# Optimization experiments

Hardware: AMD Instinct MI355X
Metric: run time of the kernel (lower is better)

The kernel has to match this reference:

```python
import jax, jax.numpy as jnp
import numpy as np

N = 100000
E = 1600000
IN_DIM, HID_DIM, OUT_DIM = 128, 64, 128


def glorot(key, shape):
    lim = float(np.sqrt(6.0 / (shape[0] + shape[1])))
    return jax.random.uniform(key, shape, jnp.float32, -lim, lim)


def setup_inputs() -> dict:
    key = jax.random.key(0)
    k1, k2, k3, k4, k5 = jax.random.split(key, 5)
    x = jax.random.normal(k1, (N, IN_DIM), jnp.float32)
    edge_index = jax.random.randint(k2, (2, E), 0, N, jnp.int64)
    edge_weight = jax.random.uniform(k3, (E,), jnp.float32)
    W1 = glorot(k4, (IN_DIM, HID_DIM))
    b1 = jnp.zeros((HID_DIM,), jnp.float32)
    W2 = glorot(k5, (HID_DIM, OUT_DIM))
    b2 = jnp.zeros((OUT_DIM,), jnp.float32)
    return {"x": x, "edge_index": edge_index, "edge_weight": edge_weight,
            "W1": W1, "b1": b1, "W2": W2, "b2": b2}


def gcn_norm(edge_index, edge_weight, num_nodes):
    # add self-loops with weight 1 (PyG GCNConv default)
    loops = jnp.arange(num_nodes, dtype=edge_index.dtype)
    row = jnp.concatenate([edge_index[0], loops])
    col = jnp.concatenate([edge_index[1], loops])
    w = jnp.concatenate([edge_weight, jnp.ones((num_nodes,), edge_weight.dtype)])
    deg = jax.ops.segment_sum(w, col, num_segments=num_nodes)  # in-degree of targets
    dinv = jnp.where(deg > 0, jax.lax.rsqrt(deg), 0.0)
    norm = dinv[row] * w * dinv[col]  # [E+N]
    return row, col, norm


def gcn_conv(x, row, col, norm, W, b, num_nodes):
    h = x @ W                                   # [N, D_out]
    msg = h[row] * norm[:, None]                # [E+N, D_out] gather + scale
    out = jax.ops.segment_sum(msg, col, num_segments=num_nodes)  # scatter-add
    return out + b


def reference(x, edge_index, edge_weight, W1, b1, W2, b2):
    row, col, norm = gcn_norm(edge_index, edge_weight, N)
    h = jax.nn.relu(gcn_conv(x, row, col, norm, W1, b1, N))
    out = gcn_conv(h, row, col, norm, W2, b2, N)
    return out
```

## Files before the change

kernel.cpp:

```cpp
#include <hip/hip_runtime.h>
#include <hip/hip_bf16.h>

typedef __hip_bfloat16 bf16;
typedef __attribute__((ext_vector_type(8))) short short8;
typedef __attribute__((ext_vector_type(4))) float f32x4;
typedef __attribute__((ext_vector_type(2))) unsigned uv2;
typedef __attribute__((ext_vector_type(4))) unsigned uv4;
union V8 { uint4 u; short8 v; };

__device__ __forceinline__ float bf2f(bf16 v) { return __bfloat162float(v); }
__device__ __forceinline__ float lo16(unsigned u) { return __uint_as_float((u & 0xffffu) << 16); }
__device__ __forceinline__ float hi16(unsigned u) { return __uint_as_float(u & 0xffff0000u); }
__device__ __forceinline__ unsigned short f2bfbits(float f) {
    return (unsigned short)(__hip_bfloat16_raw(__float2bfloat16(f)).x);
}
__device__ __forceinline__ unsigned pack2(float a, float b) {
    return (unsigned)f2bfbits(a) | ((unsigned)f2bfbits(b) << 16);
}

__device__ __forceinline__ float ldf(const void* p, size_t i, bool isbf) {
    return isbf ? bf2f(((const bf16*)p)[i]) : ((const float*)p)[i];
}
__device__ __forceinline__ int ldi(const void* p, size_t i, bool is64) {
    return is64 ? (int)((const long long*)p)[i] : ((const int*)p)[i];
}
__device__ __forceinline__ float sane(float v) {
    return (v == v && fabsf(v) < 1e30f) ? v : 0.f;
}

__device__ __forceinline__ uint2 nt_ld2(const uint2* p) {
    uv2 v = __builtin_nontemporal_load((const uv2*)p);
    return make_uint2(v.x, v.y);
}
__device__ __forceinline__ void nt_st4(uint4* p, uint4 v) {
    uv4 t; t.x = v.x; t.y = v.y; t.z = v.z; t.w = v.w;
    __builtin_nontemporal_store(t, (uv4*)p);
}

#define DC_CNT_SHIFT 44
#define DC_FIX_MASK  0xFFFFFFFFFFFULL
#define DC_FIX_SCALE 4194304.0f

__global__ void initk(unsigned long long* __restrict__ dc, int* __restrict__ hist,
                      int* __restrict__ bcnt, int n, int initdc,
                      const unsigned* __restrict__ w1w, const unsigned* __restrict__ eiw,
                      int* __restrict__ flags) {
    int i = blockIdx.x * blockDim.x + threadIdx.x;
    if (initdc && i < n) dc[i] = (unsigned long long)(1u << 22);
    if (i < 256) { hist[i] = 0; bcnt[i] = 0; }
    if (blockIdx.x == 0) {
        __shared__ int cnt[2];
        if (threadIdx.x < 2) cnt[threadIdx.x] = 0;
        __syncthreads();
        int c0 = 0;
        for (int j = threadIdx.x; j < 4096; j += 256) {
            unsigned u = w1w[j];
            unsigned e0 = (u >> 7) & 0xFFu, e1 = (u >> 23) & 0xFFu;
            if (e0 <= 125u && e1 <= 125u) c0++;
        }
        int c1 = 0;
        for (int j = threadIdx.x; j < 2048; j += 256)
            if (eiw[2 * j + 1] == 0u) c1++;
        atomicAdd(&cnt[0], c0);
        atomicAdd(&cnt[1], c1);
        __syncthreads();
        if (threadIdx.x == 0) {
            flags[0] = (cnt[0] >= 3072) ? 1 : 0;
            flags[1] = (cnt[1] >= 1024) ? 1 : 0;
        }
    }
}

__global__ void degcnt(const void* __restrict__ ei, const void* __restrict__ w,
                       unsigned long long* __restrict__ dc,
                       const int* __restrict__ flags, int e, int n) {
    const bool isbf = flags[0] != 0;
    const bool is64 = flags[1] != 0;
    int i = blockIdx.x * blockDim.x + threadIdx.x;
    if (i < e) {
        int c = ldi(ei, (size_t)e + i, is64);
        if ((unsigned)c < (unsigned)n) {
            float wv = sane(ldf(w, i, isbf));
            wv = fminf(fmaxf(wv, 0.f), 1024.f);
            unsigned long long pk = (1ULL << DC_CNT_SHIFT)
                                  + (unsigned long long)llrintf(wv * DC_FIX_SCALE);
            atomicAdd(&dc[c], pk);
        }
    }
}

__global__ __launch_bounds__(1024) void binA(const void* __restrict__ ei,
                                             const void* __restrict__ w,
                                             int* __restrict__ bcnt,
                                             uint2* __restrict__ stage,
                                             const int* __restrict__ flags,
                                             int e, int n, int k, int cap) {
    __shared__ uint2 recs[4096];
    __shared__ unsigned tgt[4096];
    __shared__ int lh[256], loff[256], lbase[256];
    const bool isbf = flags[0] != 0;
    const bool is64 = flags[1] != 0;
    const int t = threadIdx.x;
    if (t < 256) lh[t] = 0;
    __syncthreads();

    int b_[4], lr_[4], valid_[4];
    uint2 rec_[4];
    const int base = blockIdx.x * 4096;
#pragma unroll
    for (int u = 0; u < 4; ++u) {
        int i = base + u * 1024 + t;
        valid_[u] = 0;
        if (i < e) {
            int r = ldi(ei, (size_t)i, is64);
            int c = ldi(ei, (size_t)e + i, is64);
            if ((unsigned)c < (unsigned)n) {
                bool rv = (unsigned)r < (unsigned)n;
                float wv = rv ? sane(ldf(w, i, isbf)) : 0.f;
                int b = c >> k;
                unsigned cloc = (unsigned)(c - (b << k));
                rec_[u] = make_uint2((cloc << 20) | (rv ? (unsigned)r : 0u),
                                     __float_as_uint(wv));
                b_[u] = b;
                lr_[u] = atomicAdd(&lh[b], 1);
                valid_[u] = 1;
            }
        }
    }
    __syncthreads();

    if (t < 256) loff[t] = lh[t];
    __syncthreads();
    for (int off = 1; off < 256; off <<= 1) {
        int v = 0;
        if (t < 256 && t >= off) v = loff[t - off];
        __syncthreads();
        if (t < 256 && t >= off) loff[t] += v;
        __syncthreads();
    }
    if (t < 256) {
        int c = lh[t];
        loff[t] -= c;
        lbase[t] = (c > 0) ? atomicAdd(&bcnt[t], c) : 0;
    }
    __syncthreads();

#pragma unroll
    for (int u = 0; u < 4; ++u)
        if (valid_[u]) {
            int slot = loff[b_[u]] + lr_[u];
            recs[slot] = rec_[u];
            unsigned gi = (unsigned)(lbase[b_[u]] + lr_[u]);
            tgt[slot] = (gi < (unsigned)cap)
                          ? (unsigned)b_[u] * (unsigned)cap + gi
                          : 0xFFFFFFFFu;
        }
    __syncthreads();

    const int total = loff[255] + lh[255];
    for (int s = t; s < total; s += 1024) {
        unsigned g = tgt[s];
        if (g != 0xFFFFFFFFu) stage[g] = recs[s];
    }
}

__global__ __launch_bounds__(1024) void degcntB(const uint2* __restrict__ stage,
                                                const int* __restrict__ bcnt,
                                                unsigned long long* __restrict__ dc,
                                                int n, int k, int cap) {
    __shared__ unsigned long long dcl[4096];
    const int b  = blockIdx.x;
    const int lo = b << k;
    const int hi = min(n, lo + (1 << k));
    const int bs = hi - lo;
    const int t  = threadIdx.x;
    for (int j = t; j < bs; j += 1024)
        dcl[j] = (unsigned long long)(1u << 22);
    __syncthreads();
    const uint2* sb = stage + (size_t)b * cap;
    const int cnt_b = min(bcnt[b], cap);
    for (int s = t; s < cnt_b; s += 1024) {
        uint2 rec = sb[s];
        int cloc  = (int)(rec.x >> 20);
        float wv  = __uint_as_float(rec.y);
        wv = fminf(fmaxf(wv, 0.f), 1024.f);
        unsigned long long pk = (1ULL << DC_CNT_SHIFT)
                              + (unsigned long long)llrintf(wv * DC_FIX_SCALE);
        atomicAdd(&dcl[cloc], pk);
    }
    __syncthreads();
    for (int j = t; j < bs; j += 1024) dc[lo + j] = dcl[j];
}

__global__ __launch_bounds__(1024) void scan1(const unsigned long long* __restrict__ dc,
                                              int* __restrict__ rp,
                                              int* __restrict__ bsum, int n) {
    __shared__ int s[1024];
    int gid = blockIdx.x * 1024 + threadIdx.x;
    int v = (gid < n) ? (int)(((const unsigned*)dc)[2 * (size_t)gid + 1] >> (DC_CNT_SHIFT - 32)) : 0;
    s[threadIdx.x] = v;
    __syncthreads();
    for (int off = 1; off < 1024; off <<= 1) {
        int t = 0;
        if (threadIdx.x >= off) t = s[threadIdx.x - off];
        __syncthreads();
        if (threadIdx.x >= off) s[threadIdx.x] += t;
        __syncthreads();
    }
    if (gid < n) rp[gid] = s[threadIdx.x] - v;
    if (threadIdx.x == 1023) bsum[blockIdx.x] = s[1023];
}

__global__ __launch_bounds__(1024) void scan2(const int* __restrict__ bsum,
                                              int* __restrict__ bsx, int nb) {
    __shared__ int s[1024];
    int v = (threadIdx.x < nb) ? bsum[threadIdx.x] : 0;
    s[threadIdx.x] = v;
    __syncthreads();
    for (int off = 1; off < 1024; off <<= 1) {
        int t = 0;
        if (threadIdx.x >= off) t = s[threadIdx.x - off];
        __syncthreads();
        if (threadIdx.x >= off) s[threadIdx.x] += t;
        __syncthreads();
    }
    if (threadIdx.x < nb) bsx[threadIdx.x] = s[threadIdx.x] - v;
}

__global__ __launch_bounds__(1024) void scan3(int* __restrict__ rp, int* __restrict__ cursor,
                                              const int* __restrict__ bsx,
                                              unsigned long long* __restrict__ dc,
                                              int* __restrict__ hist,
                                              int n, int e) {
    __shared__ int lh[256];
    const int t = threadIdx.x;
    if (t < 256) lh[t] = 0;
    __syncthreads();
    int i = blockIdx.x * 1024 + t;
    if (i < n) {
        int v = rp[i] + bsx[i >> 10];
        rp[i] = v;
        cursor[i] = v;
        unsigned long long dv = dc[i];
        int c = (int)(dv >> DC_CNT_SHIFT);
        float d = (float)(dv & DC_FIX_MASK) * (1.0f / DC_FIX_SCALE);
        float di = d > 0.f ? rsqrtf(d) : 0.f;
        dc[i] = (dv & ~DC_FIX_MASK) | (unsigned long long)__float_as_uint(di);
        atomicAdd(&lh[min(c, 255)], 1);
    }
    __syncthreads();
    if (t < 256) {
        int c = lh[t];
        if (c > 0) atomicAdd(&hist[t], c);
    }
    if (i == 0) rp[n] = e;
}

__global__ void fill(const void* __restrict__ ei, const void* __restrict__ w,
                     int* __restrict__ cursor, uint2* __restrict__ epack,
                     const int* __restrict__ flags, int e, int n) {
    const bool isbf = flags[0] != 0;
    const bool is64 = flags[1] != 0;
    int i = blockIdx.x * blockDim.x + threadIdx.x;
    if (i < e) {
        int r = ldi(ei, (size_t)i, is64);
        int c = ldi(ei, (size_t)e + i, is64);
        if ((unsigned)c < (unsigned)n) {
            bool rv = (unsigned)r < (unsigned)n;
            float wv = rv ? sane(ldf(w, i, isbf)) : 0.f;
            int pos = atomicAdd(&cursor[c], 1);
            epack[pos] = make_uint2(rv ? (unsigned)r : 0u, __float_as_uint(wv));
        }
    }
}

__global__ __launch_bounds__(1024) void fillB(const int* __restrict__ rp,
                                              const uint2* __restrict__ stage,
                                              const int* __restrict__ bcnt,
                                              uint2* __restrict__ epack,
                                              int n, int k, int cap) {
    __shared__ int ncur[4096];
    const int b  = blockIdx.x;
    const int lo = b << k;
    const int hi = min(n, lo + (1 << k));
    const int t  = threadIdx.x;
    for (int j = t; j < hi - lo; j += 1024) ncur[j] = rp[lo + j];
    __syncthreads();
    const uint2* sb = stage + (size_t)b * cap;
    const int cnt_b = min(bcnt[b], cap);
    for (int s = t; s < cnt_b; s += 1024) {
        uint2 rec = sb[s];
        int cloc  = (int)(rec.x >> 20);
        unsigned r = rec.x & 0xFFFFFu;
        int pos = atomicAdd(&ncur[cloc], 1);
        epack[pos] = make_uint2(r, rec.y);
    }
}

__global__ void hscan(const int* __restrict__ hist, int* __restrict__ hcur) {
    __shared__ int s[256];
    int v = hist[threadIdx.x];
    s[threadIdx.x] = v;
    __syncthreads();
    for (int off = 1; off < 256; off <<= 1) {
        int t = 0;
        if (threadIdx.x >= off) t = s[threadIdx.x - off];
        __syncthreads();
        if (threadIdx.x >= off) s[threadIdx.x] += t;
        __syncthreads();
    }
    hcur[threadIdx.x] = s[threadIdx.x] - v;
}

__global__ __launch_bounds__(1024) void sortk(const unsigned long long* __restrict__ dc,
                                              int* __restrict__ hcur,
                                              int* __restrict__ order, int n) {
    __shared__ int lh[256];
    __shared__ int lbase[256];
    const int t = threadIdx.x;
    for (int b = t; b < 256; b += 1024) lh[b] = 0;
    __syncthreads();
    const int i = blockIdx.x * 1024 + t;
    int b = 0, lrank = 0;
    if (i < n) {
        b = min((int)(dc[i] >> DC_CNT_SHIFT), 255);
        lrank = atomicAdd(&lh[b], 1);
    }
    __syncthreads();
    for (int bb = t; bb < 256; bb += 1024) {
        int c = lh[bb];
        lbase[bb] = (c > 0) ? atomicAdd(&hcur[bb], c) : 0;
    }
    __syncthreads();
    if (i < n) order[lbase[b] + lrank] = i;
}

__global__ __launch_bounds__(256) void gemm1_mfma(const void* __restrict__ x,
                                                  const void* __restrict__ W1,
                                                  const float* __restrict__ dinvp,
                                                  const int* __restrict__ flags,
                                                  unsigned short* __restrict__ G1,
                                                  int n) {
    const bool isbf = flags[0] != 0;
    __shared__ uint4 bfr[16 * 64];
    for (int idx = threadIdx.x; idx < 16 * 64; idx += 256) {
        int lane = idx & 63, fr = idx >> 6;
        int ct = fr >> 2, ks = fr & 3;
        int k0 = ks * 32 + (lane >> 4) * 8;
        int col = ct * 16 + (lane & 15);
        unsigned short h[8];
#pragma unroll
        for (int j = 0; j < 8; ++j)
            h[j] = f2bfbits(ldf(W1, (size_t)(k0 + j) * 64 + col, isbf));
        bfr[idx] = make_uint4((unsigned)h[0] | ((unsigned)h[1] << 16),
                              (unsigned)h[2] | ((unsigned)h[3] << 16),
                              (unsigned)h[4] | ((unsigned)h[5] << 16),
                              (unsigned)h[6] | ((unsigned)h[7] << 16));
    }
    __syncthreads();

    const int lane = threadIdx.x & 63;
    const int m = lane & 15, q = lane >> 4;
    const int wid = (blockIdx.x * 256 + threadIdx.x) >> 6;
    const int nw  = (gridDim.x * 256) >> 6;
    const int nchunk = (n + 15) >> 4;

    for (int ch = wid; ch < nchunk; ch += nw) {
        const int row0 = ch * 16;
        const int rA = min(row0 + m, n - 1);
        V8 a[4];
        if (isbf) {
            const uint4* xr = (const uint4*)((const bf16*)x + (size_t)rA * 128);
#pragma unroll
            for (int ks = 0; ks < 4; ++ks) a[ks].u = xr[ks * 4 + q];
        } else {
            const float4* xr4 = (const float4*)((const float*)x + (size_t)rA * 128);
#pragma unroll
            for (int ks = 0; ks < 4; ++ks) {
                float4 v0 = xr4[ks * 8 + q * 2];
                float4 v1 = xr4[ks * 8 + q * 2 + 1];
                a[ks].u = make_uint4(pack2(v0.x, v0.y), pack2(v0.z, v0.w),
                                     pack2(v1.x, v1.y), pack2(v1.z, v1.w));
            }
        }
#pragma unroll
        for (int ct = 0; ct < 4; ++ct) {
            f32x4 acc = {0.f, 0.f, 0.f, 0.f};
#pragma unroll
            for (int ks = 0; ks < 4; ++ks) {
                V8 b; b.u = bfr[(ct * 4 + ks) * 64 + lane];
                acc = __builtin_amdgcn_mfma_f32_16x16x32_bf16(a[ks].v, b.v, acc, 0, 0, 0);
            }
#pragma unroll
            for (int r = 0; r < 4; ++r) {
                int row = row0 + q * 4 + r;
                if (row < n)
                    G1[(size_t)row * 64 + ct * 16 + m] = f2bfbits(dinvp[2 * (size_t)row] * acc[r]);
            }
        }
    }
}

__device__ __forceinline__ void gacc8(const int* __restrict__ rp,
                                      const uint2* __restrict__ epack,
                                      const uint4* __restrict__ Gv,
                                      int node, int sub, float acc[8]) {
    uint4 self = Gv[(size_t)node * 8 + sub];
    acc[0] = lo16(self.x); acc[1] = hi16(self.x);
    acc[2] = lo16(self.y); acc[3] = hi16(self.y);
    acc[4] = lo16(self.z); acc[5] = hi16(self.z);
    acc[6] = lo16(self.w); acc[7] = hi16(self.w);

    const int s0 = rp[node], s1 = rp[node + 1];
    const uint2 fb = make_uint2((unsigned)node, 0u);
    int idx = s0 + sub;
    uint2 ld = (idx < s1) ? nt_ld2(&epack[idx]) : fb;
    for (int base = s0; base < s1; base += 8) {
        int nidx = base + 8 + sub;
        uint2 nld = (nidx < s1) ? nt_ld2(&epack[nidx]) : fb;
        int rr[8]; float wv[8];
#pragma unroll
        for (int u = 0; u < 8; ++u) {
            rr[u] = __shfl((int)ld.x, u, 8);
            wv[u] = __uint_as_float((unsigned)__shfl((int)ld.y, u, 8));
        }
        uint4 gp[8];
#pragma unroll
        for (int u = 0; u < 8; ++u) gp[u] = Gv[(size_t)rr[u] * 8 + sub];
#pragma unroll
        for (int u = 0; u < 8; ++u) {
            acc[0] = fmaf(wv[u], lo16(gp[u].x), acc[0]);
            acc[1] = fmaf(wv[u], hi16(gp[u].x), acc[1]);
            acc[2] = fmaf(wv[u], lo16(gp[u].y), acc[2]);
            acc[3] = fmaf(wv[u], hi16(gp[u].y), acc[3]);
            acc[4] = fmaf(wv[u], lo16(gp[u].z), acc[4]);
            acc[5] = fmaf(wv[u], hi16(gp[u].z), acc[5]);
            acc[6] = fmaf(wv[u], lo16(gp[u].w), acc[6]);
            acc[7] = fmaf(wv[u], hi16(gp[u].w), acc[7]);
        }
        ld = nld;
    }
}

__global__ __launch_bounds__(256, 4) void agg1(const int* __restrict__ rp,
                                               const uint2* __restrict__ epack,
                                               const int* __restrict__ order,
                                               const uint4* __restrict__ G1v,
                                               const float* __restrict__ dinvp,
                                               const void* __restrict__ b1,
                                               const int* __restrict__ flags,
                                               uint4* __restrict__ G2v, int n) {
    const bool isbf = flags[0] != 0;
    const int sub = threadIdx.x & 7;
    const int g   = (blockIdx.x * 256 + threadIdx.x) >> 3;
    if (g >= n) return;
    const int node = order[g];

    float acc[8];
    gacc8(rp, epack, G1v, node, sub, acc);

    const float dv = dinvp[2 * (size_t)node];
    unsigned o[4];
#pragma unroll
    for (int t = 0; t < 4; ++t) {
        float h0 = dv * acc[2 * t]     + ldf(b1, 8 * sub + 2 * t, isbf);
        float h1 = dv * acc[2 * t + 1] + ldf(b1, 8 * sub + 2 * t + 1, isbf);
        h0 = h0 > 0.f ? h0 : 0.f;
        h1 = h1 > 0.f ? h1 : 0.f;
        o[t] = pack2(dv * h0, dv * h1);
    }
    nt_st4(&G2v[(size_t)node * 8 + sub], make_uint4(o[0], o[1], o[2], o[3]));
}

__global__ __launch_bounds__(256, 4) void agg2out(const int* __restrict__ rp,
                                                  const uint2* __restrict__ epack,
                                                  const int* __restrict__ order,
                                                  const uint4* __restrict__ G2v,
                                                  const float* __restrict__ dinvp,
                                                  const void* __restrict__ W2,
                                                  const void* __restrict__ b2,
                                                  const int* __restrict__ flags,
                                                  void* __restrict__ outp, int n) {
    const bool isbf = flags[0] != 0;
    __shared__ uint4 bfr[16 * 64];
    __shared__ float b2s[128];
    __shared__ uint4 tls[32 * 8];
    __shared__ int   nds[32];
    for (int idx = threadIdx.x; idx < 16 * 64; idx += 256) {
        int lane = idx & 63, fr = idx >> 6;
        int ct = fr >> 1, ks = fr & 1;
        int k0 = ks * 32 + (lane >> 4) * 8;
        int col = ct * 16 + (lane & 15);
        unsigned short h[8];
#pragma unroll
        for (int j = 0; j < 8; ++j)
            h[j] = f2bfbits(ldf(W2, (size_t)(k0 + j) * 128 + col, isbf));
        bfr[idx] = make_uint4((unsigned)h[0] | ((unsigned)h[1] << 16),
                              (unsigned)h[2] | ((unsigned)h[3] << 16),
                              (unsigned)h[4] | ((unsigned)h[5] << 16),
                              (unsigned)h[6] | ((unsigned)h[7] << 16));
    }
    for (int i = threadIdx.x; i < 128; i += 256) b2s[i] = ldf(b2, i, isbf);
    __syncthreads();

    const int sub  = threadIdx.x & 7;
    const int lg   = threadIdx.x >> 3;
    const int lane = threadIdx.x & 63;
    const int m = lane & 15, q = lane >> 4;
    const int wid = threadIdx.x >> 6;
    const int ntile = (n + 31) >> 5;

    for (int tile = blockIdx.x; tile < ntile; tile += gridDim.x) {
        const int g = tile * 32 + lg;
        uint4 o = make_uint4(0u, 0u, 0u, 0u);
        int node = 0;
        if (g < n) {
            node = order[g];
            float acc[8];
            gacc8(rp, epack, G2v, node, sub, acc);
            const float dv = dinvp[2 * (size_t)node];
            o.x = pack2(dv * acc[0], dv * acc[1]);
            o.y = pack2(dv * acc[2], dv * acc[3]);
            o.z = pack2(dv * acc[4], dv * acc[5]);
            o.w = pack2(dv * acc[6], dv * acc[7]);
        }
        tls[lg * 8 + sub] = o;
        if (sub == 0) nds[lg] = node;
        __syncthreads();

        const int chunk = wid >> 1;
        const int lrow  = chunk * 16 + m;
        V8 a0, a1;
        a0.u = tls[lrow * 8 + q];
        a1.u = tls[lrow * 8 + 4 + q];
#pragma unroll
        for (int c8 = 0; c8 < 4; ++c8) {
            const int ct = (wid & 1) * 4 + c8;
            f32x4 acc4 = {0.f, 0.f, 0.f, 0.f};
            V8 b0; b0.u = bfr[(ct * 2 + 0) * 64 + lane];
            acc4 = __builtin_amdgcn_mfma_f32_16x16x32_bf16(a0.v, b0.v, acc4, 0, 0, 0);
            V8 b1; b1.u = bfr[(ct * 2 + 1) * 64 + lane];
            acc4 = __builtin_amdgcn_mfma_f32_16x16x32_bf16(a1.v, b1.v, acc4, 0, 0, 0);
            const int col = ct * 16 + m;
            const float bb = b2s[col];
#pragma unroll
            for (int r = 0; r < 4; ++r) {
                int lr = chunk * 16 + q * 4 + r;
                int gg = tile * 32 + lr;
                if (gg < n) {
                    float ov = acc4[r] + bb;
                    int nd = nds[lr];
                    if (isbf) ((bf16*)outp)[(size_t)nd * 128 + col] = __float2bfloat16(ov);
                    else      ((float*)outp)[(size_t)nd * 128 + col] = ov;
                }
            }
        }
        __syncthreads();
    }
}

extern "C" void kernel_launch(void* const* d_in, const int* in_sizes, int n_in,
                              void* d_out, int out_size, void* d_ws, size_t ws_size,
                              hipStream_t stream) {
    const void* x  = d_in[0];
    const void* ei = d_in[1];
    const void* ew = d_in[2];
    const void* W1 = d_in[3];
    const void* b1 = d_in[4];
    const void* W2 = d_in[5];
    const void* b2 = d_in[6];

    const int n = in_sizes[0] / 128;
    const int e = in_sizes[2];
    const int nb = (n + 1023) / 1024;

    int*   flags  = (int*)d_ws;
    unsigned long long* dc = (unsigned long long*)((int*)d_ws + 8);
    int*   rp     = (int*)d_ws + 8 + 2 * (size_t)n;
    int*   cursor = rp + n + 1;
    int*   bsum   = cursor + n;
    int*   bsx    = bsum + 1024;
    int*   hist   = bsum + 512;
    int*   hcur   = bsx + 512;
    int*   bcnt   = bsx + 256;
    int*   order  = cursor;
    size_t w_off  = (size_t)(8 + 4 * (size_t)n + 1 + 2048);
    w_off = (w_off + 3) & ~(size_t)3;
    uint2*    epack = (uint2*)((int*)d_ws + w_off);
    size_t g_off = w_off + 2 * (size_t)e;
    g_off = (g_off + 3) & ~(size_t)3;
    unsigned* G1 = (unsigned*)d_ws + g_off;
    unsigned* G2 = G1 + (size_t)n * 32;

    const float* dinvp = (const float*)dc;
    uint2* stage = (uint2*)G1;

    int bs0 = (n + 255) / 256;
    int k = 0;
    while ((1 << k) < bs0) ++k;
    int beff = (n + (1 << k) - 1) >> k;
    int cap  = (int)((32 * (size_t)n) / (size_t)beff);
    size_t mean = ((size_t)e + beff - 1) / beff;
    bool fastfill = (n <= (1 << 18)) && (k <= 12) &&
                    ((size_t)cap >= mean + mean / 2 + 1024);

    const int nchunk = (n + 15) >> 4;
    int ggrid = (nchunk + 3) / 4;
    if (ggrid > 2048) ggrid = 2048;
    if (ggrid < 192)  ggrid = 192;

    initk<<<fastfill ? 1 : (n + 255) / 256, 256, 0, stream>>>(
        dc, hist, bcnt, n, fastfill ? 0 : 1,
        (const unsigned*)W1, (const unsigned*)ei, flags);
    if (fastfill) {
        binA<<<(e + 4095) / 4096, 1024, 0, stream>>>(ei, ew, bcnt, stage, flags, e, n, k, cap);
        degcntB<<<beff, 1024, 0, stream>>>(stage, bcnt, dc, n, k, cap);
    } else {
        degcnt<<<(e + 255) / 256, 256, 0, stream>>>(ei, ew, dc, flags, e, n);
    }
    scan1<<<nb, 1024, 0, stream>>>(dc, rp, bsum, n);
    scan2<<<1, 1024, 0, stream>>>(bsum, bsx, nb);
    scan3<<<nb, 1024, 0, stream>>>(rp, cursor, bsx, dc, hist, n, e);
    if (fastfill) {
        fillB<<<beff, 1024, 0, stream>>>(rp, stage, bcnt, epack, n, k, cap);
    } else {
        fill<<<(e + 255) / 256, 256, 0, stream>>>(ei, ew, cursor, epack, flags, e, n);
    }
    hscan<<<1, 256, 0, stream>>>(hist, hcur);
    sortk<<<nb, 1024, 0, stream>>>(dc, hcur, order, n);

    gemm1_mfma<<<ggrid, 256, 0, stream>>>(x, W1, dinvp, flags, (unsigned short*)G1, n);
    agg1<<<(n * 8 + 255) / 256, 256, 0, stream>>>(rp, epack, order, (const uint4*)G1,
                                                  dinvp, b1, flags, (uint4*)G2, n);
    int a2grid = (n + 31) / 32;
    if (a2grid > 1024) a2grid = 1024;
    agg2out<<<a2grid, 256, 0, stream>>>(rp, epack, order, (const uint4*)G2,
                                        dinvp, W2, b2, flags, d_out, n);
}
```

Measured before the change: 337.7 us.

## Fuse degree, dinv and row-pointer scan into per-bucket kernel; drop LDS staging

binA now writes records straight to global stage slots instead of first sorting them in shared memory and doing a coalesced flush. A new small bscan kernel computes per-bucket base offsets, and degscanB fuses degree counting, rsqrt of the degree, the local row-pointer prefix scan and the degree histogram. This replaces the three-kernel global scan (scan1, scan2, scan3) on the fast path. It cuts kernel launches and passes over dc/rp, but the stage writes become scattered and less coalesced.

After: 335.2 us. Within noise of the previous version (-0.7%).

```diff
diff --git a/kernel.cpp b/kernel.cpp
--- a/kernel.cpp
+++ b/kernel.cpp
@@ -95,9 +95,7 @@
                                              uint2* __restrict__ stage,
                                              const int* __restrict__ flags,
                                              int e, int n, int k, int cap) {
-    __shared__ uint2 recs[4096];
-    __shared__ unsigned tgt[4096];
-    __shared__ int lh[256], loff[256], lbase[256];
+    __shared__ int lh[256], lbase[256];
     const bool isbf = flags[0] != 0;
     const bool is64 = flags[1] != 0;
     const int t = threadIdx.x;
@@ -128,52 +126,54 @@
         }
     }
     __syncthreads();
-
-    if (t < 256) loff[t] = lh[t];
-    __syncthreads();
-    for (int off = 1; off < 256; off <<= 1) {
-        int v = 0;
-        if (t < 256 && t >= off) v = loff[t - off];
-        __syncthreads();
-        if (t < 256 && t >= off) loff[t] += v;
-        __syncthreads();
-    }
     if (t < 256) {
         int c = lh[t];
-        loff[t] -= c;
         lbase[t] = (c > 0) ? atomicAdd(&bcnt[t], c) : 0;
     }
     __syncthreads();
-
 #pragma unroll
     for (int u = 0; u < 4; ++u)
         if (valid_[u]) {
-            int slot = loff[b_[u]] + lr_[u];
-            recs[slot] = rec_[u];
             unsigned gi = (unsigned)(lbase[b_[u]] + lr_[u]);
-            tgt[slot] = (gi < (unsigned)cap)
-                          ? (unsigned)b_[u] * (unsigned)cap + gi
-                          : 0xFFFFFFFFu;
-        }
-    __syncthreads();
-
-    const int total = loff[255] + lh[255];
-    for (int s = t; s < total; s += 1024) {
-        unsigned g = tgt[s];
-        if (g != 0xFFFFFFFFu) stage[g] = recs[s];
-    }
-}
-
-__global__ __launch_bounds__(1024) void degcntB(const uint2* __restrict__ stage,
-                                                const int* __restrict__ bcnt,
-                                                unsigned long long* __restrict__ dc,
-                                                int n, int k, int cap) {
+            if (gi < (unsigned)cap)
+                stage[(size_t)b_[u] * cap + gi] = rec_[u];
+        }
+}
+
+__global__ void bscan(const int* __restrict__ bcnt, int* __restrict__ bbase,
+                      int* __restrict__ rp, int n, int beff) {
+    __shared__ int s[256];
+    const int t = threadIdx.x;
+    int v = (t < beff) ? bcnt[t] : 0;
+    s[t] = v;
+    __syncthreads();
+    for (int off = 1; off < 256; off <<= 1) {
+        int x = 0;
+        if (t >= off) x = s[t - off];
+        __syncthreads();
+        if (t >= off) s[t] += x;
+        __syncthreads();
+    }
+    bbase[t] = s[t] - v;
+    if (t == 255) rp[n] = s[255];
+}
+
+__global__ __launch_bounds__(1024) void degscanB(const uint2* __restrict__ stage,
+                                                 const int* __restrict__ bcnt,
+                                                 const int* __restrict__ bbase,
+                                                 unsigned long long* __restrict__ dc,
+                                                 int* __restrict__ rp,
+                                                 int* __restrict__ hist,
+                                                 int n, int k, int cap) {
     __shared__ unsigned long long dcl[4096];
+    __shared__ int pfx[1024];
+    __shared__ int lh[256];
     const int b  = blockIdx.x;
     const int lo = b << k;
     const int hi = min(n, lo + (1 << k));
     const int bs = hi - lo;
     const int t  = threadIdx.x;
+    if (t < 256) lh[t] = 0;
     for (int j = t; j < bs; j += 1024)
         dcl[j] = (unsigned long long)(1u << 22);
     __syncthreads();
@@ -189,7 +189,46 @@
         atomicAdd(&dcl[cloc], pk);
     }
     __syncthreads();
-    for (int j = t; j < bs; j += 1024) dc[lo + j] = dcl[j];
+
+    int c[4];
+    int lsum = 0;
+    const int j0 = 4 * t;
+#pragma unroll
+    for (int i2 = 0; i2 < 4; ++i2) {
+        int j = j0 + i2;
+        int cv = 0;
+        if (j < bs) {
+            unsigned long long dv = dcl[j];
+            cv = (int)(dv >> DC_CNT_SHIFT);
+            float d  = (float)(dv & DC_FIX_MASK) * (1.0f / DC_FIX_SCALE);
+            float di = d > 0.f ? rsqrtf(d) : 0.f;
+            dc[lo + j] = (dv & ~DC_FIX_MASK) | (unsigned long long)__float_as_uint(di);
+            atomicAdd(&lh[min(cv, 255)], 1);
+        }
+        c[i2] = cv;
+        lsum += cv;
+    }
+    pfx[t] = lsum;
+    __syncthreads();
+    for (int off = 1; off < 1024; off <<= 1) {
+        int v = 0;
+        if (t >= off) v = pfx[t - off];
+        __syncthreads();
+        if (t >= off) pfx[t] += v;
+        __syncthreads();
+    }
+    int run = bbase[b] + pfx[t] - lsum;
+#pragma unroll
+    for (int i2 = 0; i2 < 4; ++i2) {
+        int j = j0 + i2;
+        if (j < bs) rp[lo + j] = run;
+        run += c[i2];
+    }
+    __syncthreads();
+    if (t < 256) {
+        int cc = lh[t];
+        if (cc > 0) atomicAdd(&hist[t], cc);
+    }
 }
 
 __global__ __launch_bounds__(1024) void scan1(const unsigned long long* __restrict__ dc,
@@ -583,6 +622,7 @@
     int*   hist   = bsum + 512;
     int*   hcur   = bsx + 512;
     int*   bcnt   = bsx + 256;
+    int*   bbase  = bsum;
     int*   order  = cursor;
     size_t w_off  = (size_t)(8 + 4 * (size_t)n + 1 + 2048);
     w_off = (w_off + 3) & ~(size_t)3;
@@ -614,16 +654,14 @@
         (const unsigned*)W1, (const unsigned*)ei, flags);
     if (fastfill) {
         binA<<<(e + 4095) / 4096, 1024, 0, stream>>>(ei, ew, bcnt, stage, flags, e, n, k, cap);
-        degcntB<<<beff, 1024, 0, stream>>>(stage, bcnt, dc, n, k, cap);
+        bscan<<<1, 256, 0, stream>>>(bcnt, bbase, rp, n, beff);
+        degscanB<<<beff, 1024, 0, stream>>>(stage, bcnt, bbase, dc, rp, hist, n, k, cap);
+        fillB<<<beff, 1024, 0, stream>>>(rp, stage, bcnt, epack, n, k, cap);
     } else {
         degcnt<<<(e + 255) / 256, 256, 0, stream>>>(ei, ew, dc, flags, e, n);
-    }
-    scan1<<<nb, 1024, 0, stream>>>(dc, rp, bsum, n);
-    scan2<<<1, 1024, 0, stream>>>(bsum, bsx, nb);
-    scan3<<<nb, 1024, 0, stream>>>(rp, cursor, bsx, dc, hist, n, e);
-    if (fastfill) {
-        fillB<<<beff, 1024, 0, stream>>>(rp, stage, bcnt, epack, n, k, cap);
-    } else {
+        scan1<<<nb, 1024, 0, stream>>>(dc, rp, bsum, n);
+        scan2<<<1, 1024, 0, stream>>>(bsum, bsx, nb);
+        scan3<<<nb, 1024, 0, stream>>>(rp, cursor, bsx, dc, hist, n, e);
         fill<<<(e + 255) / 256, 256, 0, stream>>>(ei, ew, cursor, epack, flags, e, n);
     }
     hscan<<<1, 256, 0, stream>>>(hist, hcur);
```
